# Kernel optimization log

Measured on AMD Instinct MI355X. Metric: run time of the kernel, lower is better.

## Reference

```python
import jax, jax.numpy as jnp
import numpy as np

D_MODEL = 1024
N_HEADS = 16
L = 2048
S = 2048
B = 4


def setup_inputs() -> dict:
    key = jax.random.key(0)
    ks = jax.random.split(key, 12)
    std = 0.02
    inp = {
        "query": jax.random.normal(ks[0], (L, B, D_MODEL), dtype=jnp.float32),
        "key": jax.random.normal(ks[1], (S, B, D_MODEL), dtype=jnp.float32),
        "value": jax.random.normal(ks[2], (S, B, D_MODEL), dtype=jnp.float32),
        # True = masked (matches torch masked_fill semantics); causal mask
        "attn_mask": jnp.triu(jnp.ones((L, S), dtype=bool), k=1),
        "Wq": std * jax.random.normal(ks[3], (D_MODEL, D_MODEL), dtype=jnp.float32),
        "bq": jnp.zeros((D_MODEL,), dtype=jnp.float32),
        "Wk": std * jax.random.normal(ks[4], (D_MODEL, D_MODEL), dtype=jnp.float32),
        "bk": jnp.zeros((D_MODEL,), dtype=jnp.float32),
        "Wv": std * jax.random.normal(ks[5], (D_MODEL, D_MODEL), dtype=jnp.float32),
        "bv": jnp.zeros((D_MODEL,), dtype=jnp.float32),
        "Wo": std * jax.random.normal(ks[6], (D_MODEL, D_MODEL), dtype=jnp.float32),
        "bo": jnp.zeros((D_MODEL,), dtype=jnp.float32),
    }
    return inp


def reference(query, key, value, attn_mask, Wq, bq, Wk, bk, Wv, bv, Wo, bo):
    Lq, Bb, D = query.shape
    H = N_HEADS
    dh = D // H
    # NOTE: module uses d_model**-0.5 (not d_qkv**-0.5)
    scale = D ** (-0.5)
    Q = (query @ Wq.T + bq).reshape(Lq, Bb, H, dh)
    K = (key @ Wk.T + bk).reshape(-1, Bb, H, dh)
    V = (value @ Wv.T + bv).reshape(-1, Bb, H, dh)
    # scores: (L, S, B, H)
    scores = jnp.einsum('ibnd,jbnd->ijbn', Q, K) * scale
    scores = jnp.where(attn_mask[:, :, None, None], -jnp.inf, scores)
    attn_weights = jax.nn.softmax(scores, axis=1)  # softmax over key axis j
    # dropout in eval mode -> identity
    out = jnp.einsum('ijbn,jbnd->ibnd', attn_weights, V).reshape(Lq, Bb, D)
    out = out @ Wo.T + bo
    return out
```

## Files before the change

### kernel.cpp

```cpp
#include <hip/hip_runtime.h>
#include <hip/hip_bf16.h>

typedef __hip_bfloat16 bf16;
typedef __attribute__((ext_vector_type(8))) short short8;
typedef __attribute__((ext_vector_type(8))) __bf16 bf16x8;
typedef __attribute__((ext_vector_type(4))) float f32x4;
typedef __attribute__((ext_vector_type(2))) unsigned int u32x2;

#define L_CTX 2048
#define B_SZ 4
#define DM 1024
#define NH 16
#define DH 64
#define M_ROWS (L_CTX * B_SZ)
#define SCQ 0.04508422002778011f

__device__ __forceinline__ void load_lds16(const void* g, void* l) {
  __builtin_amdgcn_global_load_lds(
      (const __attribute__((address_space(1))) unsigned int*)g,
      (__attribute__((address_space(3))) unsigned int*)l, 16, 0, 0);
}

__device__ __forceinline__ f32x4 mfma16(short8 a, short8 b, f32x4 c) {
  return __builtin_amdgcn_mfma_f32_16x16x32_bf16(
      __builtin_bit_cast(bf16x8, a), __builtin_bit_cast(bf16x8, b), c, 0, 0, 0);
}

__device__ __forceinline__ short tobf(float x) {
  return __builtin_bit_cast(short, __float2bfloat16(x));
}

__device__ __forceinline__ short tobf_rh(float x) {
  unsigned u = __builtin_bit_cast(unsigned, x);
  return (short)((u + 0x8000u) >> 16);
}

#if __has_builtin(__builtin_amdgcn_exp2f)
#define EXP2(x) __builtin_amdgcn_exp2f(x)
#else
#define EXP2(x) exp2f(x)
#endif

#if __has_builtin(__builtin_amdgcn_rcpf)
#define RCP(x) __builtin_amdgcn_rcpf(x)
#else
#define RCP(x) (1.0f / (x))
#endif

#define TRRD(d, N) \
  asm volatile("ds_read_b64_tr_b16 %0, %1 offset:" #N : "=v"(d) : "v"(va))

__device__ __forceinline__ short8 mkv(u32x2 a, u32x2 b) {
  union { unsigned u[4]; short8 s; } x;
  x.u[0] = a.x; x.u[1] = a.y; x.u[2] = b.x; x.u[3] = b.y;
  return x.s;
}

__global__ void cast_all(const float* __restrict__ q, const float* __restrict__ k,
                         const float* __restrict__ v, const float* __restrict__ wq,
                         const float* __restrict__ wk, const float* __restrict__ wv,
                         const float* __restrict__ wo, bf16* __restrict__ dq,
                         bf16* __restrict__ dk, bf16* __restrict__ dv,
                         bf16* __restrict__ dwq, bf16* __restrict__ dwk,
                         bf16* __restrict__ dwv, bf16* __restrict__ dwo) {
  unsigned u = blockIdx.x * 256u + threadIdx.x;
  const float* src;
  bf16* dst;
  unsigned off;
  if (u < 3145728u) {
    unsigned which = u >> 20;
    off = u & 1048575u;
    src = which == 0 ? q : which == 1 ? k : v;
    dst = which == 0 ? dq : which == 1 ? dk : dv;
  } else {
    unsigned w = u - 3145728u;
    unsigned which = w >> 17;
    off = w & 131071u;
    src = which == 0 ? wq : which == 1 ? wk : which == 2 ? wv : wo;
    dst = which == 0 ? dwq : which == 1 ? dwk : which == 2 ? dwv : dwo;
  }
  const float4* s4 = (const float4*)src + (size_t)off * 2;
  float4 a = s4[0], b = s4[1];
  union { bf16 h[8]; short8 s; } o;
  o.h[0] = __float2bfloat16(a.x); o.h[1] = __float2bfloat16(a.y);
  o.h[2] = __float2bfloat16(a.z); o.h[3] = __float2bfloat16(a.w);
  o.h[4] = __float2bfloat16(b.x); o.h[5] = __float2bfloat16(b.y);
  o.h[6] = __float2bfloat16(b.z); o.h[7] = __float2bfloat16(b.w);
  *(short8*)(dst + (size_t)off * 8) = o.s;
}

template <int MODE>
__device__ __forceinline__ void gemm_body(const bf16* __restrict__ A,
                                          const bf16* __restrict__ Bw,
                                          const float* __restrict__ bias,
                                          void* __restrict__ Cout, float scale,
                                          int bxi, int byi) {
  const int K = DM, N = DM;
  const int tid = threadIdx.x;
  const int wv = tid >> 6, ln = tid & 63, g = ln >> 4, lc = ln & 15;
  const int wr = wv >> 1, wc = wv & 1;
  const int bm = byi * 128, bn = bxi * 128;

  __shared__ char smem[49152];

  f32x4 acc[4][4] = {};

  const int srow = tid >> 2, sc_ = tid & 3;
  auto stage = [&](int t, int s) {
    int kk = t * 32;
#pragma unroll
    for (int i = 0; i < 2; ++i) {
      int row = i * 64 + srow;
      int cs = sc_ ^ (row & 3);
      load_lds16(A + (size_t)(bm + row) * K + kk + cs * 8,
                 smem + s * 16384 + i * 4096 + wv * 1024);
      load_lds16(Bw + (size_t)(bn + row) * K + kk + cs * 8,
                 smem + s * 16384 + 8192 + i * 4096 + wv * 1024);
    }
  };

  stage(0, 0);
  stage(1, 1);
  asm volatile("s_waitcnt vmcnt(4)" ::: "memory");
  __syncthreads();

#pragma unroll
  for (int t = 0; t < 32; ++t) {
    if (t + 2 < 32) stage(t + 2, (t + 2) % 3);
    const char* As = smem + (t % 3) * 16384;
    const char* Bs = As + 8192;
    short8 af[4], bfr[4];
#pragma unroll
    for (int m = 0; m < 4; ++m)
      af[m] = *(const short8*)(As + (wr * 64 + m * 16 + lc) * 64 +
                               ((g ^ (lc & 3)) << 4));
#pragma unroll
    for (int n = 0; n < 4; ++n)
      bfr[n] = *(const short8*)(Bs + (wc * 64 + n * 16 + lc) * 64 +
                                ((g ^ (lc & 3)) << 4));
    __builtin_amdgcn_s_setprio(1);
#pragma unroll
    for (int m = 0; m < 4; ++m)
#pragma unroll
      for (int n = 0; n < 4; ++n) acc[m][n] = mfma16(af[m], bfr[n], acc[m][n]);
    __builtin_amdgcn_s_setprio(0);
    if (t + 2 < 32)
      asm volatile("s_waitcnt vmcnt(4)" ::: "memory");
    else
      asm volatile("s_waitcnt vmcnt(0)" ::: "memory");
    __syncthreads();
  }

#pragma unroll
  for (int n = 0; n < 4; ++n) {
    int col = bn + wc * 64 + n * 16 + lc;
    float bv = bias[col];
#pragma unroll
    for (int m = 0; m < 4; ++m) {
      int row0 = bm + wr * 64 + m * 16 + g * 4;
#pragma unroll
      for (int i = 0; i < 4; ++i) {
        int row = row0 + i;
        float val = (acc[m][n][i] + bv) * scale;
        if (MODE == 0) {
          int l = row >> 2, b = row & 3, h = col >> 6, d = col & 63;
          ((bf16*)Cout)[(((size_t)(b * NH + h)) * L_CTX + l) * DH + d] =
              __float2bfloat16(val);
        } else {
          ((float*)Cout)[(size_t)row * N + col] = val;
        }
      }
    }
  }
}

__global__ __launch_bounds__(256, 3) void gemm_qkv(
    const bf16* __restrict__ Aq, const bf16* __restrict__ Ak,
    const bf16* __restrict__ Av, const bf16* __restrict__ Wq,
    const bf16* __restrict__ Wk, const bf16* __restrict__ Wv,
    const float* __restrict__ bq, const float* __restrict__ bk,
    const float* __restrict__ bv, bf16* __restrict__ Oq, bf16* __restrict__ Ok,
    bf16* __restrict__ Ov) {
  int bid = blockIdx.x;
  int xcd = bid & 7, t = bid >> 3;
  int u = t >> 3, bx = t & 7;
  int gma = xcd * 24 + u;
  int by = gma & 63, z = gma >> 6;
  const bf16* A = z == 0 ? Aq : z == 1 ? Ak : Av;
  const bf16* W = z == 0 ? Wq : z == 1 ? Wk : Wv;
  const float* bs = z == 0 ? bq : z == 1 ? bk : bv;
  bf16* O = z == 0 ? Oq : z == 1 ? Ok : Ov;
  float sc = z == 0 ? SCQ : 1.0f;
  gemm_body<0>(A, W, bs, O, sc, bx, by);
}

__global__ __launch_bounds__(256, 3) void gemm_out(const bf16* __restrict__ A,
                                                   const bf16* __restrict__ Bw,
                                                   const float* __restrict__ bias,
                                                   float* __restrict__ Cout) {
  int bid = blockIdx.x;
  int xcd = bid & 7, t = bid >> 3;
  int u = t >> 3, bx = t & 7;
  int by = xcd * 8 + u;
  gemm_body<1>(A, Bw, bias, Cout, 1.0f, bx, by);
}

__global__ __launch_bounds__(256, 4) void attn_fwd7(const bf16* __restrict__ Q,
                                                    const bf16* __restrict__ K,
                                                    const bf16* __restrict__ V,
                                                    bf16* __restrict__ O) {
  const int tid = threadIdx.x, w = tid >> 6, ln = tid & 63, g = ln >> 4,
            lc = ln & 15;
  const int bid = blockIdx.x;
  const int j = bid >> 3;
  const int bh = (bid & 7) * 8 + (j & 7);
  const int pa = j >> 3;
  const int b = bh >> 4, h = bh & 15;

  __shared__ char smem[32768];
  const bf16* Qh = Q + (size_t)bh * L_CTX * DH;
  const bf16* Kh = K + (size_t)bh * L_CTX * DH;
  const bf16* Vh = V + (size_t)bh * L_CTX * DH;

  const unsigned vbase =
      (unsigned)(size_t)(__attribute__((address_space(3))) char*)(smem + 16384);

  const int krow_l = ln >> 3, kslot = ln & 7;
  const int vr = (ln & 7) >> 1, vc0 = (ln & 1) * 8;

  const short ONEBF = 0x3F80;
  const short8 ones8 = {ONEBF, ONEBF, ONEBF, ONEBF, ONEBF, ONEBF, ONEBF, ONEBF};

#pragma unroll 1
  for (int rep = 0; rep < 2; ++rep) {
    const int qt = rep ? (31 - pa) : pa;
    const int qb = qt * 64 + w * 16;
    const int nt = qt + 1;

    short8 qf0 = *(const short8*)(Qh + (qb + lc) * DH + g * 8);
    short8 qf1 = *(const short8*)(Qh + (qb + lc) * DH + 32 + g * 8);

    f32x4 oacc[4] = {};
    f32x4 lacc = {};

    auto stage = [&](int t, int s) {
#pragma unroll
      for (int i = 0; i < 2; ++i) {
        int row = (i * 4 + w) * 8 + krow_l;
        int slot = kslot ^ (row & 7);
        load_lds16(Kh + (size_t)(t * 64 + row) * DH + slot * 8,
                   smem + s * 8192 + (i * 4 + w) * 1024);
      }
#pragma unroll
      for (int Lg = 0; Lg < 2; ++Lg) {
        int blk = w * 8 + Lg * 32 + krow_l;
        int sq = blk & 15, dt = blk >> 4;
        load_lds16(Vh + (size_t)(t * 64 + sq * 4 + vr) * DH + dt * 16 + vc0,
                   smem + 16384 + s * 8192 + Lg * 4096 + w * 1024);
      }
    };

    int sel = 0;
    stage(0, 0);
    asm volatile("s_waitcnt vmcnt(0)" ::: "memory");
    __syncthreads();

    for (int t = 0; t < nt; ++t) {
      if (t + 1 < nt) stage(t + 1, sel ^ 1);

      const char* Kl = smem + sel * 8192;
      f32x4 st[4] = {};
      __builtin_amdgcn_s_setprio(1);
#pragma unroll
      for (int tt = 0; tt < 4; ++tt) {
        int row = tt * 16 + lc, sw = lc & 7;
        short8 kf0 = *(const short8*)(Kl + row * 128 + ((g ^ sw) << 4));
        short8 kf1 = *(const short8*)(Kl + row * 128 + (((4 + g) ^ sw) << 4));
        st[tt] = mfma16(kf0, qf0, st[tt]);
        st[tt] = mfma16(kf1, qf1, st[tt]);
      }
      __builtin_amdgcn_s_setprio(0);

      unsigned va = vbase + sel * 8192 + ln * 8;
      u32x2 t0a, t0b, t1a, t1b, t2a, t2b, t3a, t3b;
      u32x2 s0a, s0b, s1a, s1b, s2a, s2b, s3a, s3b;
      TRRD(t0a, 0);    TRRD(t0b, 512);
      TRRD(t1a, 2048); TRRD(t1b, 2560);
      TRRD(t2a, 4096); TRRD(t2b, 4608);
      TRRD(t3a, 6144); TRRD(t3b, 6656);
      TRRD(s0a, 1024); TRRD(s0b, 1536);
      TRRD(s1a, 3072); TRRD(s1b, 3584);
      TRRD(s2a, 5120); TRRD(s2b, 5632);
      TRRD(s3a, 7168); TRRD(s3b, 7680);

      if (t == nt - 1) {
        int qrel = w * 16 + lc;
#pragma unroll
        for (int tt = 0; tt < 4; ++tt)
#pragma unroll
          for (int i = 0; i < 4; ++i)
            if (tt * 16 + g * 4 + i > qrel) st[tt][i] = -__builtin_inff();
      }

      union { short s[8]; short8 v; } p0, p1;
#pragma unroll
      for (int i = 0; i < 4; ++i) {
        p0.s[i]     = tobf_rh(EXP2(st[0][i]));
        p0.s[4 + i] = tobf_rh(EXP2(st[1][i]));
        p1.s[i]     = tobf_rh(EXP2(st[2][i]));
        p1.s[4 + i] = tobf_rh(EXP2(st[3][i]));
      }

      asm volatile("s_waitcnt lgkmcnt(0)" ::: "memory");
      __builtin_amdgcn_sched_barrier(0);
      __builtin_amdgcn_s_setprio(1);
      oacc[0] = mfma16(p0.v, mkv(t0a, t0b), oacc[0]);
      oacc[1] = mfma16(p0.v, mkv(t1a, t1b), oacc[1]);
      oacc[2] = mfma16(p0.v, mkv(t2a, t2b), oacc[2]);
      oacc[3] = mfma16(p0.v, mkv(t3a, t3b), oacc[3]);
      lacc = mfma16(p0.v, ones8, lacc);
      oacc[0] = mfma16(p1.v, mkv(s0a, s0b), oacc[0]);
      oacc[1] = mfma16(p1.v, mkv(s1a, s1b), oacc[1]);
      oacc[2] = mfma16(p1.v, mkv(s2a, s2b), oacc[2]);
      oacc[3] = mfma16(p1.v, mkv(s3a, s3b), oacc[3]);
      lacc = mfma16(p1.v, ones8, lacc);
      __builtin_amdgcn_s_setprio(0);

      asm volatile("s_waitcnt vmcnt(0)" ::: "memory");
      __syncthreads();
      sel ^= 1;
    }

    float li[4];
#pragma unroll
    for (int i = 0; i < 4; ++i) li[i] = RCP(lacc[i]);
#pragma unroll
    for (int n = 0; n < 4; ++n)
#pragma unroll
      for (int i = 0; i < 4; ++i) {
        int qi = qb + g * 4 + i;
        int col = h * DH + n * 16 + lc;
        O[((size_t)qi * B_SZ + b) * DM + col] =
            __float2bfloat16(oacc[n][i] * li[i]);
      }
  }
}

extern "C" void kernel_launch(void* const* d_in, const int* in_sizes, int n_in,
                              void* d_out, int out_size, void* d_ws, size_t ws_size,
                              hipStream_t stream) {
  const float* q = (const float*)d_in[0];
  const float* k = (const float*)d_in[1];
  const float* v = (const float*)d_in[2];
  const float* wq = (const float*)d_in[4];
  const float* bq = (const float*)d_in[5];
  const float* wk = (const float*)d_in[6];
  const float* bk = (const float*)d_in[7];
  const float* wv = (const float*)d_in[8];
  const float* bv = (const float*)d_in[9];
  const float* wo = (const float*)d_in[10];
  const float* bo = (const float*)d_in[11];

  if (ws_size < 125829120u) return;

  char* ws = (char*)d_ws;
  bf16* qb_ = (bf16*)(ws);
  bf16* kb_ = (bf16*)(ws + 16777216);
  bf16* vb_ = (bf16*)(ws + 33554432);
  bf16* wqb = (bf16*)(ws + 50331648);
  bf16* wkb = (bf16*)(ws + 52428800);
  bf16* wvb = (bf16*)(ws + 54525952);
  bf16* wob = (bf16*)(ws + 56623104);
  bf16* Qp = (bf16*)(ws + 58720256);
  bf16* Kp = (bf16*)(ws + 75497472);
  bf16* Vp = (bf16*)(ws + 92274688);
  bf16* Ob = (bf16*)(ws + 109051904);

  cast_all<<<14336, 256, 0, stream>>>(q, k, v, wq, wk, wv, wo, qb_, kb_, vb_, wqb,
                                      wkb, wvb, wob);
  gemm_qkv<<<1536, 256, 0, stream>>>(qb_, kb_, vb_, wqb, wkb, wvb, bq, bk, bv,
                                     Qp, Kp, Vp);
  attn_fwd7<<<1024, 256, 0, stream>>>(Qp, Kp, Vp, Ob);
  gemm_out<<<512, 256, 0, stream>>>(Ob, wob, bo, (float*)d_out);
}
```

Before: 158.4 us.

## Use 256x256 tiles with 8 waves for QKV projection GEMM

Replaces the shared templated GEMM body with a dedicated QKV kernel that uses 256x256 output tiles, 512 threads, 8 waves each computing 128x64, and double-buffered LDS staging. The larger tile raises arithmetic intensity and cuts global reloads of A and W. The price is more registers per wave and lower occupancy, and the pipeline is only two stages deep with a full vmcnt(0) wait every step. It also changes the LDS swizzle to XOR with (row>>1)&3 in both GEMMs to reduce bank conflicts, and specializes gemm_out into its own kernel.

Result: slower. 166.1 us (+4.9%).

```diff
diff --git a/kernel.cpp b/kernel.cpp
--- a/kernel.cpp
+++ b/kernel.cpp
@@ -89,13 +89,106 @@
   *(short8*)(dst + (size_t)off * 8) = o.s;
 }
 
-template <int MODE>
-__device__ __forceinline__ void gemm_body(const bf16* __restrict__ A,
-                                          const bf16* __restrict__ Bw,
-                                          const float* __restrict__ bias,
-                                          void* __restrict__ Cout, float scale,
-                                          int bxi, int byi) {
+__global__ __launch_bounds__(512, 2) void gemm_qkv(
+    const bf16* __restrict__ Aq, const bf16* __restrict__ Ak,
+    const bf16* __restrict__ Av, const bf16* __restrict__ Wq,
+    const bf16* __restrict__ Wk, const bf16* __restrict__ Wv,
+    const float* __restrict__ bq, const float* __restrict__ bk,
+    const float* __restrict__ bv, bf16* __restrict__ Oq, bf16* __restrict__ Ok,
+    bf16* __restrict__ Ov) {
+  const int K = DM;
+  int bid = blockIdx.x;
+  int xcd = bid & 7, t_ = bid >> 3;
+  int z = t_ >> 4, rem = t_ & 15;
+  int bx = rem & 3, by = xcd * 4 + (rem >> 2);
+  const bf16* A = z == 0 ? Aq : z == 1 ? Ak : Av;
+  const bf16* W = z == 0 ? Wq : z == 1 ? Wk : Wv;
+  const float* bias = z == 0 ? bq : z == 1 ? bk : bv;
+  bf16* Cout = z == 0 ? Oq : z == 1 ? Ok : Ov;
+  const float scale = z == 0 ? SCQ : 1.0f;
+
+  const int tid = threadIdx.x;
+  const int wid = tid >> 6, ln = tid & 63, g = ln >> 4, lc = ln & 15;
+  const int wm = wid >> 2, wn = wid & 3;
+  const int bm = by * 256, bn = bx * 256;
+
+  __shared__ char smem[65536];
+
+  f32x4 acc[8][4] = {};
+
+  auto stage = [&](int t, int s) {
+    int kk = t * 32;
+#pragma unroll
+    for (int l = 0; l < 4; ++l) {
+      int idx = (l & 1) * 512 + tid;
+      int rowi = idx >> 2, chunk = idx & 3;
+      int cs = chunk ^ ((rowi >> 1) & 3);
+      char* dst = smem + s * 32768 + (l >> 1) * 16384 + (l & 1) * 8192 +
+                  wid * 1024 + ln * 16;
+      if (l < 2)
+        load_lds16(A + (size_t)(bm + rowi) * K + kk + cs * 8, dst);
+      else
+        load_lds16(W + (size_t)(bn + rowi) * K + kk + cs * 8, dst);
+    }
+  };
+
+  stage(0, 0);
+  asm volatile("s_waitcnt vmcnt(0)" ::: "memory");
+  __syncthreads();
+
+  for (int t = 0; t < 32; ++t) {
+    if (t + 1 < 32) stage(t + 1, (t + 1) & 1);
+    const char* As = smem + (t & 1) * 32768;
+    const char* Bs = As + 16384;
+    short8 af[8], bfr[4];
+#pragma unroll
+    for (int m = 0; m < 8; ++m) {
+      int row = wm * 128 + m * 16 + lc;
+      af[m] = *(const short8*)(As + row * 64 + ((g ^ ((row >> 1) & 3)) << 4));
+    }
+#pragma unroll
+    for (int n = 0; n < 4; ++n) {
+      int row = wn * 64 + n * 16 + lc;
+      bfr[n] = *(const short8*)(Bs + row * 64 + ((g ^ ((row >> 1) & 3)) << 4));
+    }
+    __builtin_amdgcn_s_setprio(1);
+#pragma unroll
+    for (int m = 0; m < 8; ++m)
+#pragma unroll
+      for (int n = 0; n < 4; ++n) acc[m][n] = mfma16(af[m], bfr[n], acc[m][n]);
+    __builtin_amdgcn_s_setprio(0);
+    asm volatile("s_waitcnt vmcnt(0)" ::: "memory");
+    __syncthreads();
+  }
+
+#pragma unroll
+  for (int n = 0; n < 4; ++n) {
+    int col = bn + wn * 64 + n * 16 + lc;
+    float bv = bias[col];
+    int h = col >> 6, d = col & 63;
+#pragma unroll
+    for (int m = 0; m < 8; ++m) {
+      int row0 = bm + wm * 128 + m * 16 + g * 4;
+#pragma unroll
+      for (int i = 0; i < 4; ++i) {
+        int row = row0 + i;
+        int l = row >> 2, b = row & 3;
+        Cout[(((size_t)(b * NH + h)) * L_CTX + l) * DH + d] =
+            __float2bfloat16((acc[m][n][i] + bv) * scale);
+      }
+    }
+  }
+}
+
+__global__ __launch_bounds__(256, 3) void gemm_out(const bf16* __restrict__ A,
+                                                   const bf16* __restrict__ Bw,
+                                                   const float* __restrict__ bias,
+                                                   float* __restrict__ Cout) {
   const int K = DM, N = DM;
+  int bid = blockIdx.x;
+  int xcd = bid & 7, t_ = bid >> 3;
+  int u = t_ >> 3, bxi = t_ & 7;
+  int byi = xcd * 8 + u;
   const int tid = threadIdx.x;
   const int wv = tid >> 6, ln = tid & 63, g = ln >> 4, lc = ln & 15;
   const int wr = wv >> 1, wc = wv & 1;
@@ -111,7 +204,7 @@
 #pragma unroll
     for (int i = 0; i < 2; ++i) {
       int row = i * 64 + srow;
-      int cs = sc_ ^ (row & 3);
+      int cs = sc_ ^ ((row >> 1) & 3);
       load_lds16(A + (size_t)(bm + row) * K + kk + cs * 8,
                  smem + s * 16384 + i * 4096 + wv * 1024);
       load_lds16(Bw + (size_t)(bn + row) * K + kk + cs * 8,
@@ -131,13 +224,15 @@
     const char* Bs = As + 8192;
     short8 af[4], bfr[4];
 #pragma unroll
-    for (int m = 0; m < 4; ++m)
-      af[m] = *(const short8*)(As + (wr * 64 + m * 16 + lc) * 64 +
-                               ((g ^ (lc & 3)) << 4));
-#pragma unroll
-    for (int n = 0; n < 4; ++n)
-      bfr[n] = *(const short8*)(Bs + (wc * 64 + n * 16 + lc) * 64 +
-                                ((g ^ (lc & 3)) << 4));
+    for (int m = 0; m < 4; ++m) {
+      int row = wr * 64 + m * 16 + lc;
+      af[m] = *(const short8*)(As + row * 64 + ((g ^ ((row >> 1) & 3)) << 4));
+    }
+#pragma unroll
+    for (int n = 0; n < 4; ++n) {
+      int row = wc * 64 + n * 16 + lc;
+      bfr[n] = *(const short8*)(Bs + row * 64 + ((g ^ ((row >> 1) & 3)) << 4));
+    }
     __builtin_amdgcn_s_setprio(1);
 #pragma unroll
     for (int m = 0; m < 4; ++m)
@@ -161,48 +256,10 @@
 #pragma unroll
       for (int i = 0; i < 4; ++i) {
         int row = row0 + i;
-        float val = (acc[m][n][i] + bv) * scale;
-        if (MODE == 0) {
-          int l = row >> 2, b = row & 3, h = col >> 6, d = col & 63;
-          ((bf16*)Cout)[(((size_t)(b * NH + h)) * L_CTX + l) * DH + d] =
-              __float2bfloat16(val);
-        } else {
-          ((float*)Cout)[(size_t)row * N + col] = val;
-        }
-      }
-    }
-  }
-}
-
-__global__ __launch_bounds__(256, 3) void gemm_qkv(
-    const bf16* __restrict__ Aq, const bf16* __restrict__ Ak,
-    const bf16* __restrict__ Av, const bf16* __restrict__ Wq,
-    const bf16* __restrict__ Wk, const bf16* __restrict__ Wv,
-    const float* __restrict__ bq, const float* __restrict__ bk,
-    const float* __restrict__ bv, bf16* __restrict__ Oq, bf16* __restrict__ Ok,
-    bf16* __restrict__ Ov) {
-  int bid = blockIdx.x;
-  int xcd = bid & 7, t = bid >> 3;
-  int u = t >> 3, bx = t & 7;
-  int gma = xcd * 24 + u;
-  int by = gma & 63, z = gma >> 6;
-  const bf16* A = z == 0 ? Aq : z == 1 ? Ak : Av;
-  const bf16* W = z == 0 ? Wq : z == 1 ? Wk : Wv;
-  const float* bs = z == 0 ? bq : z == 1 ? bk : bv;
-  bf16* O = z == 0 ? Oq : z == 1 ? Ok : Ov;
-  float sc = z == 0 ? SCQ : 1.0f;
-  gemm_body<0>(A, W, bs, O, sc, bx, by);
-}
-
-__global__ __launch_bounds__(256, 3) void gemm_out(const bf16* __restrict__ A,
-                                                   const bf16* __restrict__ Bw,
-                                                   const float* __restrict__ bias,
-                                                   float* __restrict__ Cout) {
-  int bid = blockIdx.x;
-  int xcd = bid & 7, t = bid >> 3;
-  int u = t >> 3, bx = t & 7;
-  int by = xcd * 8 + u;
-  gemm_body<1>(A, Bw, bias, Cout, 1.0f, bx, by);
+        Cout[(size_t)row * N + col] = acc[m][n][i] + bv;
+      }
+    }
+  }
 }
 
 __global__ __launch_bounds__(256, 4) void attn_fwd7(const bf16* __restrict__ Q,
@@ -378,8 +435,8 @@
 
   cast_all<<<14336, 256, 0, stream>>>(q, k, v, wq, wk, wv, wo, qb_, kb_, vb_, wqb,
                                       wkb, wvb, wob);
-  gemm_qkv<<<1536, 256, 0, stream>>>(qb_, kb_, vb_, wqb, wkb, wvb, bq, bk, bv,
-                                     Qp, Kp, Vp);
+  gemm_qkv<<<384, 512, 0, stream>>>(qb_, kb_, vb_, wqb, wkb, wvb, bq, bk, bv,
+                                    Qp, Kp, Vp);
   attn_fwd7<<<1024, 256, 0, stream>>>(Qp, Kp, Vp, Ob);
   gemm_out<<<512, 256, 0, stream>>>(Ob, wob, bo, (float*)d_out);
 }
```
